# Performance work log

Hardware: AMD Instinct MI355X
Metric: run time of the kernel (lower is better)

## Reference

```python
import jax, jax.numpy as jnp
import numpy as np

B, Cin, Cout, H, W, K = 8, 256, 256, 64, 64, 3  # kernel 3x3, stride 1, pad 1, dilation 1
EPS = 1e-5


def setup_inputs() -> dict:
    key = jax.random.key(0)
    k0, k1, k2 = jax.random.split(key, 3)
    x = jax.random.normal(k0, (B, Cin, H, W), jnp.float32)
    # offset-predicting conv (mmcv zero-inits it; use small random weights so offsets are nontrivial)
    w_off = jax.random.normal(k1, (2 * K * K, Cin, K, K), jnp.float32) * 0.01
    b_off = jnp.zeros((2 * K * K,), jnp.float32)
    # main deformable conv weight
    w = jax.random.normal(k2, (Cout, Cin, K, K), jnp.float32) * (1.0 / np.sqrt(Cin * K * K))
    b = jnp.zeros((Cout,), jnp.float32)
    gamma = jnp.ones((Cout,), jnp.float32)
    beta = jnp.zeros((Cout,), jnp.float32)
    return {"x": x, "w_off": w_off, "b_off": b_off, "w": w, "b": b, "gamma": gamma, "beta": beta}


def _deform_fusion(x, w_off, b_off, w, b, gamma, beta):
    Bn, C, Hh, Ww = x.shape
    # 1) predict offsets: [B, 2*K*K, H, W]; channel layout is (dy, dx) per kernel tap
    offset = jax.lax.conv_general_dilated(x, w_off, (1, 1), ((1, 1), (1, 1)))
    offset = offset + b_off[None, :, None, None]
    off = offset.reshape(Bn, K * K, 2, Hh, Ww)
    dy, dx = off[:, :, 0], off[:, :, 1]  # each [B, K*K, H, W]

    # 2) sampling positions: p = p0 + p_k + delta_p  (stride 1, pad 1 -> p_k in {-1,0,1})
    kk = jnp.arange(K * K)
    ky = (kk // K - (K // 2)).astype(jnp.float32)[None, :, None, None]
    kx = (kk % K - (K // 2)).astype(jnp.float32)[None, :, None, None]
    py = ky + jnp.arange(Hh, dtype=jnp.float32)[None, None, :, None] + dy  # [B,K2,H,W]
    px = kx + jnp.arange(Ww, dtype=jnp.float32)[None, None, None, :] + dx

    # 3) bilinear sampling with zero padding outside the image
    y0 = jnp.floor(py); x0 = jnp.floor(px)
    fy = py - y0; fx = px - x0
    x_flat = x.reshape(Bn, C, Hh * Ww)

    def corner(yi, xi, wgt):
        valid = (yi >= 0) & (yi <= Hh - 1) & (xi >= 0) & (xi <= Ww - 1)
        idx = (jnp.clip(yi, 0, Hh - 1) * Ww + jnp.clip(xi, 0, Ww - 1)).astype(jnp.int32)
        idx = idx.reshape(Bn, -1)  # [B, K2*H*W]
        g = jax.vmap(lambda xf, ii: jnp.take(xf, ii, axis=1))(x_flat, idx)  # [B,C,K2*H*W]
        return g * (wgt * valid).reshape(Bn, 1, -1)

    sampled = (corner(y0,     x0,     (1 - fy) * (1 - fx))
             + corner(y0,     x0 + 1, (1 - fy) * fx)
             + corner(y0 + 1, x0,     fy * (1 - fx))
             + corner(y0 + 1, x0 + 1, fy * fx))  # [B, C, K2*H*W]
    sampled = sampled.reshape(Bn, C, K * K, Hh * Ww)

    # 4) contract sampled patches with conv weight: implicit-GEMM of deformable conv
    out = jnp.einsum('bckp,ock->bop', sampled, w.reshape(w.shape[0], C, K * K))
    out = out + b[None, :, None]
    out = out.reshape(Bn, -1, Hh, Ww)

    # 5) BatchNorm (training-mode batch statistics) + ReLU
    mean = out.mean(axis=(0, 2, 3), keepdims=True)
    var = out.var(axis=(0, 2, 3), keepdims=True)
    out = gamma[None, :, None, None] * (out - mean) * jax.lax.rsqrt(var + EPS) + beta[None, :, None, None]
    return jax.nn.relu(out)


def reference(x, w_off, b_off, w, b, gamma, beta):
    return _deform_fusion(x, w_off, b_off, w, b, gamma, beta)
```

## Files before the change

kernel.cpp:

```cpp
#include <hip/hip_runtime.h>
#include <math.h>

#define BN_ 8
#define CIN 256
#define COUT 256
#define HH 64
#define WW 64
#define HW 4096
#define KK 9
#define OC 18
#define EPS 1e-5f
#define NTOT (BN_ * COUT * HW)

#define OFF_WS 0
#define WTB_WS 589824
#define WOB_WS 884736
#define ST_WS  921600
#define XT_WS  922112

typedef float f32x4 __attribute__((ext_vector_type(4)));
typedef float f32x2 __attribute__((ext_vector_type(2)));
typedef short s16x8 __attribute__((ext_vector_type(8)));
typedef unsigned int u32x4 __attribute__((ext_vector_type(4)));

__device__ __forceinline__ unsigned short f2bf(float f) {
  unsigned int u = __float_as_uint(f);
  unsigned int r = (u + 0x7fffu + ((u >> 16) & 1u)) >> 16;
  return (unsigned short)r;
}
__device__ __forceinline__ float bf2f(short s) {
  return __uint_as_float(((unsigned int)(unsigned short)s) << 16);
}

__global__ __launch_bounds__(256) void xpose_kernel(
    const float* __restrict__ x, unsigned short* __restrict__ xt) {
  __shared__ float s[64][65];
  const int t = threadIdx.x;
  const int p0 = blockIdx.x * 64;
  const int c0 = blockIdx.y * 64;
  const int b  = blockIdx.z;
  const float* xb = x + ((size_t)b * CIN + c0) * HW + p0;
#pragma unroll
  for (int pass = 0; pass < 4; ++pass) {
    int cr = pass * 16 + (t >> 4);
    int ps = (t & 15) * 4;
    float4 v = *(const float4*)(xb + (size_t)cr * HW + ps);
    s[ps + 0][cr] = v.x; s[ps + 1][cr] = v.y; s[ps + 2][cr] = v.z; s[ps + 3][cr] = v.w;
  }
  __syncthreads();
  unsigned short* xo = xt + (size_t)b * 32 * HW * 8;
#pragma unroll
  for (int r = 0; r < 2; ++r) {
    int flat = r * 256 + t;
    int pr = flat >> 3, sub = flat & 7;
    int g8 = (c0 >> 3) + sub;
    s16x8 v;
#pragma unroll
    for (int j = 0; j < 8; ++j) v[j] = (short)f2bf(s[pr][sub * 8 + j]);
    *(s16x8*)(xo + ((size_t)g8 * HW + p0 + pr) * 8) = v;
  }
}

__global__ __launch_bounds__(256) void prep_kernel(
    const float* __restrict__ w_off, const float* __restrict__ w,
    unsigned short* __restrict__ wob, unsigned short* __restrict__ wTb,
    float* __restrict__ stats) {
  const int kb = blockIdx.x;
  const int kk = kb >> 3;
  const int c0 = (kb & 7) << 5;
  const int t = threadIdx.x;
  if (kb == 71) { stats[t] = 0.f; stats[256 + t] = 0.f; }
#pragma unroll
  for (int r = 0; r < 4; ++r) {
    int e = r * 256 + t;
    int g = e >> 8, m = (e >> 3) & 31, j = e & 7;
    int c = c0 + g * 8 + j;
    unsigned short v = 0;
    if (m < OC) v = f2bf(w_off[((size_t)m * CIN + c) * 9 + kk]);
    wob[(size_t)kb * 1024 + e] = v;
  }
#pragma unroll
  for (int g = 0; g < 4; ++g)
#pragma unroll
    for (int j = 0; j < 8; ++j) {
      int c = c0 + g * 8 + j;
      wTb[(((size_t)kb * 4 + g) * 256 + t) * 8 + j] =
          f2bf(w[((size_t)t * CIN + c) * 9 + kk]);
    }
}

__global__ __launch_bounds__(512, 4) void gemm_kernel(
    const unsigned short* __restrict__ xt, const unsigned short* __restrict__ wTb,
    const unsigned short* __restrict__ wob, const float* __restrict__ b_off,
    const float* __restrict__ bias, float* __restrict__ out,
    float* __restrict__ stats) {
  __shared__ __align__(16) char lds[73728];
  const int t = threadIdx.x;
  const int lane = t & 63;
  const int wv = t >> 6;
  const int b = blockIdx.x & 7;
  const int h = blockIdx.x >> 3;
  const int p0 = h * 64;
  const int col = t & 63;
  const int oct = t >> 6;
  const int fr = lane & 15, fq = lane >> 4;
  const unsigned short* xtb = xt + (size_t)b * 32 * HW * 8;
  float* s_off = (float*)(lds + 65536);
  unsigned short (*s_b)[4096] = (unsigned short(*)[4096])lds;

  {
    unsigned short* sb = (unsigned short*)lds + wv * 2048;
    f32x4 acc_o[2][4] = {};

    auto fetch = [&](int s, s16x8* V, s16x8* AF) {
      const int ki = wv * 9 + s;
      const int kk = ki >> 3, cc0g = (ki & 7) << 2;
      const int ky = kk / 3 - 1, kx = kk % 3 - 1;
      const int y = h + ky;
      const int xcol = lane + kx;
      const bool ok = (y >= 0) && (y < HH) && (xcol >= 0) && (xcol < WW);
      const int pix = y * WW + xcol;
#pragma unroll
      for (int g = 0; g < 4; ++g) {
        s16x8 v = {0, 0, 0, 0, 0, 0, 0, 0};
        if (ok)
          __builtin_memcpy(&v, (const char*)xtb + (((size_t)(cc0g + g)) << 16) + (size_t)pix * 16, 16);
        V[g] = v;
      }
      const unsigned short* ap = wob + (size_t)ki * 1024;
#pragma unroll
      for (int i = 0; i < 2; ++i)
        AF[i] = *(const s16x8*)&ap[(fq * 32 + i * 16 + fr) * 8];
    };

    s16x8 VE[4], VO[4], afE2[2], afO2[2];
    fetch(0, VE, afE2);

#define OBODY(S, VC, VN, AFC, AFN)                                             \
    {                                                                          \
      _Pragma("unroll")                                                        \
      for (int g = 0; g < 4; ++g)                                              \
        *(s16x8*)&sb[(g * 64 + lane) * 8] = VC[g];                             \
      if ((S) + 1 < 9) fetch((S) + 1, VN, AFN);                                \
      s16x8 bf[4];                                                             \
      _Pragma("unroll")                                                        \
      for (int jn = 0; jn < 4; ++jn)                                           \
        bf[jn] = *(const s16x8*)&sb[(fq * 64 + jn * 16 + fr) * 8];             \
      _Pragma("unroll")                                                        \
      for (int i = 0; i < 2; ++i)                                              \
        _Pragma("unroll")                                                      \
        for (int jn = 0; jn < 4; ++jn)                                         \
          acc_o[i][jn] = __builtin_amdgcn_mfma_f32_16x16x32_bf16(              \
              AFC[i], bf[jn], acc_o[i][jn], 0, 0, 0);                          \
    }

    for (int sp = 0; sp < 4; ++sp) {
      OBODY(2 * sp, VE, VO, afE2, afO2)
      OBODY(2 * sp + 1, VO, VE, afO2, afE2)
    }
    OBODY(8, VE, VO, afE2, afO2)
#undef OBODY

    __syncthreads();
    float* red = (float*)lds;
#pragma unroll
    for (int i = 0; i < 2; ++i)
#pragma unroll
      for (int jn = 0; jn < 4; ++jn)
#pragma unroll
        for (int rg = 0; rg < 4; ++rg)
          red[wv * 2048 + (i * 16 + fq * 4 + rg) * 64 + jn * 16 + fr] = acc_o[i][jn][rg];
    __syncthreads();

    const int e4 = t * 4;
    const int m = e4 >> 6;
    float4 v = make_float4(0.f, 0.f, 0.f, 0.f);
#pragma unroll
    for (int w = 0; w < 8; ++w) {
      float4 a = *(float4*)&red[w * 2048 + e4];
      v.x += a.x; v.y += a.y; v.z += a.z; v.w += a.w;
    }
    float bo = (m < OC) ? b_off[m] : 0.f;
    v.x += bo; v.y += bo; v.z += bo; v.w += bo;
    *(float4*)&s_off[e4] = v;
    __syncthreads();
  }

  int cofs[4];
  f32x2 qw2[4];

  auto calc = [&](int kk) {
    float dy = s_off[(2 * kk) * 64 + col];
    float dx = s_off[(2 * kk + 1) * 64 + col];
    float py = (float)(kk / 3 - 1 + h) + dy;
    float pxx = (float)(kk % 3 - 1 + col) + dx;
    float y0f = floorf(py), x0f = floorf(pxx);
    float fy = py - y0f, fx = pxx - x0f;
    int y0 = (int)y0f, x0 = (int)x0f;
    int y1 = y0 + 1, x1 = x0 + 1;
    bool vy0 = (y0 >= 0) && (y0 < HH), vy1 = (y1 >= 0) && (y1 < HH);
    bool vx0 = (x0 >= 0) && (x0 < WW), vx1 = (x1 >= 0) && (x1 < WW);
    int cy0 = min(max(y0, 0), HH - 1), cy1 = min(max(y1, 0), HH - 1);
    int cx0 = min(max(x0, 0), WW - 1), cx1 = min(max(x1, 0), WW - 1);
    float q0 = (vy0 && vx0) ? (1.f - fy) * (1.f - fx) : 0.f;
    float q1 = (vy0 && vx1) ? (1.f - fy) * fx : 0.f;
    float q2 = (vy1 && vx0) ? fy * (1.f - fx) : 0.f;
    float q3 = (vy1 && vx1) ? fy * fx : 0.f;
    cofs[0] = (cy0 * WW + cx0) * 16;  qw2[0][0] = q0; qw2[0][1] = q0;
    cofs[1] = (cy0 * WW + cx1) * 16;  qw2[1][0] = q1; qw2[1][1] = q1;
    cofs[2] = (cy1 * WW + cx0) * 16;  qw2[2][0] = q2; qw2[2][1] = q2;
    cofs[3] = (cy1 * WW + cx1) * 16;  qw2[3][0] = q3; qw2[3][1] = q3;
  };

  s16x8 g[4];

  auto gather = [&](int chunk64) {
    const char* bp = (const char*)xtb + (((size_t)(chunk64 * 8 + oct)) << 16);
#pragma unroll
    for (int k = 0; k < 4; ++k)
      __builtin_memcpy(&g[k], bp + cofs[k], 16);
  };

  auto combine_write = [&](int buf) {
    u32x4 vout;
#pragma unroll
    for (int jp = 0; jp < 4; ++jp) {
      f32x2 a = {0.f, 0.f};
#pragma unroll
      for (int k = 0; k < 4; ++k) {
        unsigned int pr = ((const unsigned int*)&g[k])[jp];
        f32x2 xv;
        xv[0] = __uint_as_float(pr << 16);
        xv[1] = __uint_as_float(pr & 0xffff0000u);
        a = __builtin_elementwise_fma(qw2[k], xv, a);
      }
      unsigned int packed;
      asm("v_cvt_pk_bf16_f32 %0, %1, %2" : "=v"(packed) : "v"(a[0]), "v"(a[1]));
      vout[jp] = packed;
    }
    *(u32x4*)&s_b[buf][(oct * 64 + col) * 8] = vout;
  };

  auto load_a = [&](int iter, s16x8 af[2][2]) {
#pragma unroll
    for (int ks = 0; ks < 2; ++ks) {
      const unsigned short* ap =
          wTb + (((size_t)(iter * 2 + ks) * 4 + fq) * 256 + wv * 32 + fr) * 8;
#pragma unroll
      for (int i = 0; i < 2; ++i)
        af[ks][i] = *(const s16x8*)(ap + (size_t)i * 16 * 8);
    }
  };

  f32x4 acc[2][4] = {};
  s16x8 afE[2][2], afO[2][2];

  {
    calc(0);
    gather(0);
    load_a(0, afE);
    combine_write(0);
  }
  asm volatile("s_waitcnt lgkmcnt(0)" ::: "memory");
  __builtin_amdgcn_s_barrier();

#define GBODY(I, AFC, AFN, CUR)                                                \
  {                                                                            \
    const int nx1 = (I) + 1;                                                   \
    if (nx1 < 36) {                                                            \
      if ((nx1 & 3) == 0) calc(nx1 >> 2);                                      \
      gather(nx1 & 3);                                                         \
      load_a(nx1, AFN);                                                        \
    }                                                                          \
    __builtin_amdgcn_s_setprio(1);                                             \
    _Pragma("unroll")                                                          \
    for (int ks = 0; ks < 2; ++ks)                                             \
      _Pragma("unroll")                                                        \
      for (int jj = 0; jj < 4; ++jj) {                                         \
        s16x8 bfr = *(const s16x8*)&s_b[CUR][((ks * 4 + fq) * 64 + jj * 16 + fr) * 8]; \
        _Pragma("unroll")                                                      \
        for (int ii = 0; ii < 2; ++ii)                                         \
          acc[ii][jj] = __builtin_amdgcn_mfma_f32_16x16x32_bf16(               \
              AFC[ks][ii], bfr, acc[ii][jj], 0, 0, 0);                         \
      }                                                                        \
    __builtin_amdgcn_s_setprio(0);                                             \
    if (nx1 < 36) {                                                            \
      combine_write((CUR) ^ 1);                                                \
      asm volatile("s_waitcnt lgkmcnt(0)" ::: "memory");                       \
      __builtin_amdgcn_s_barrier();                                            \
    }                                                                          \
  }

  for (int m = 0; m < 18; ++m) {
    const int i0 = 2 * m;
    GBODY(i0, afE, afO, 0)
    GBODY(i0 + 1, afO, afE, 1)
  }
#undef GBODY

#pragma unroll
  for (int i = 0; i < 2; ++i) {
#pragma unroll
    for (int rg = 0; rg < 4; ++rg) {
      int o = wv * 32 + i * 16 + fq * 4 + rg;
      float bv = bias[o];
      float* op = out + ((size_t)(b * COUT + o)) * HW + p0 + fr;
      float s = 0.f, s2 = 0.f;
#pragma unroll
      for (int j = 0; j < 4; ++j) {
        float val = acc[i][j][rg] + bv;
        op[j * 16] = val;
        s += val; s2 += val * val;
      }
#pragma unroll
      for (int m2 = 1; m2 < 16; m2 <<= 1) {
        s += __shfl_xor(s, m2);
        s2 += __shfl_xor(s2, m2);
      }
      if (fr == 0) {
        atomicAdd(&stats[o], s);
        atomicAdd(&stats[COUT + o], s2);
      }
    }
  }
}

__global__ __launch_bounds__(256) void bn_kernel(
    float* __restrict__ out, const float* __restrict__ stats,
    const float* __restrict__ gamma, const float* __restrict__ beta) {
  int i4 = (blockIdx.x * 256 + threadIdx.x) * 4;
  int o = (i4 >> 12) & (COUT - 1);
  const float inv_n = 1.f / (float)(BN_ * HW);
  float mean = stats[o] * inv_n;
  float var = stats[COUT + o] * inv_n - mean * mean;
  float sc = gamma[o] * rsqrtf(var + EPS);
  float sh = beta[o] - mean * sc;
  float4 v = *(float4*)(out + i4);
  v.x = fmaxf(fmaf(v.x, sc, sh), 0.f);
  v.y = fmaxf(fmaf(v.y, sc, sh), 0.f);
  v.z = fmaxf(fmaf(v.z, sc, sh), 0.f);
  v.w = fmaxf(fmaf(v.w, sc, sh), 0.f);
  *(float4*)(out + i4) = v;
}

extern "C" void kernel_launch(void* const* d_in, const int* in_sizes, int n_in,
                              void* d_out, int out_size, void* d_ws, size_t ws_size,
                              hipStream_t stream) {
  const float* x     = (const float*)d_in[0];
  const float* w_off = (const float*)d_in[1];
  const float* b_off = (const float*)d_in[2];
  const float* w     = (const float*)d_in[3];
  const float* bias  = (const float*)d_in[4];
  const float* gamma = (const float*)d_in[5];
  const float* beta  = (const float*)d_in[6];
  float* out = (float*)d_out;
  float* ws = (float*)d_ws;
  unsigned short* wTb = (unsigned short*)(ws + WTB_WS);
  unsigned short* wob = (unsigned short*)(ws + WOB_WS);
  float* stats = ws + ST_WS;
  unsigned short* xt = (unsigned short*)(ws + XT_WS);

  xpose_kernel<<<dim3(64, 4, 8), 256, 0, stream>>>(x, xt);
  prep_kernel<<<72, 256, 0, stream>>>(w_off, w, wob, wTb, stats);
  gemm_kernel<<<512, 512, 0, stream>>>(xt, wTb, wob, b_off, bias, out, stats);
  bn_kernel<<<NTOT / 1024, 256, 0, stream>>>(out, stats, gamma, beta);
}
```

Before: 213.7 us.

## Process two image rows per block with 1024 threads in the fused deform GEMM

Each block now covers two output rows (128 pixels) instead of one, using 16 waves and 256 blocks. Each wave owns 16 output channels across 128 pixels rather than 32 channels across 64 pixels. The offset-conv stage runs two passes, one per row half, and the shared sample buffer doubles. The aim is to halve the number of barrier-separated block iterations and amortize the weight loads over more pixels. In exchange, 256 blocks may underfill the CUs, LDS use grows, and launch_bounds(1024,4) is unrealistic and may constrain registers.

```diff
diff --git a/kernel.cpp b/kernel.cpp
--- a/kernel.cpp
+++ b/kernel.cpp
@@ -12,7 +12,6 @@
 #define EPS 1e-5f
 #define NTOT (BN_ * COUT * HW)
 
-#define OFF_WS 0
 #define WTB_WS 589824
 #define WOB_WS 884736
 #define ST_WS  921600
@@ -89,34 +88,37 @@
     }
 }
 
-__global__ __launch_bounds__(512, 4) void gemm_kernel(
+__global__ __launch_bounds__(1024, 4) void gemm_kernel(
     const unsigned short* __restrict__ xt, const unsigned short* __restrict__ wTb,
     const unsigned short* __restrict__ wob, const float* __restrict__ b_off,
     const float* __restrict__ bias, float* __restrict__ out,
     float* __restrict__ stats) {
-  __shared__ __align__(16) char lds[73728];
+  __shared__ __align__(16) char lds[81920];
   const int t = threadIdx.x;
   const int lane = t & 63;
   const int wv = t >> 6;
   const int b = blockIdx.x & 7;
-  const int h = blockIdx.x >> 3;
-  const int p0 = h * 64;
-  const int col = t & 63;
-  const int oct = t >> 6;
+  const int hh2 = blockIdx.x >> 3;
+  const int p0 = hh2 * 128;
+  const int col = t & 127;
+  const int oct = t >> 7;
   const int fr = lane & 15, fq = lane >> 4;
   const unsigned short* xtb = xt + (size_t)b * 32 * HW * 8;
   float* s_off = (float*)(lds + 65536);
-  unsigned short (*s_b)[4096] = (unsigned short(*)[4096])lds;
+  unsigned short (*s_b)[8192] = (unsigned short(*)[8192])lds;
 
   {
+    const int wg = wv & 7;
+    const int half = wv >> 3;
+    const int yrow = 2 * hh2 + half;
     unsigned short* sb = (unsigned short*)lds + wv * 2048;
     f32x4 acc_o[2][4] = {};
 
     auto fetch = [&](int s, s16x8* V, s16x8* AF) {
-      const int ki = wv * 9 + s;
+      const int ki = wg * 9 + s;
       const int kk = ki >> 3, cc0g = (ki & 7) << 2;
       const int ky = kk / 3 - 1, kx = kk % 3 - 1;
-      const int y = h + ky;
+      const int y = yrow + ky;
       const int xcol = lane + kx;
       const bool ok = (y >= 0) && (y < HH) && (xcol >= 0) && (xcol < WW);
       const int pix = y * WW + xcol;
@@ -164,36 +166,44 @@
     __syncthreads();
     float* red = (float*)lds;
 #pragma unroll
-    for (int i = 0; i < 2; ++i)
-#pragma unroll
-      for (int jn = 0; jn < 4; ++jn)
-#pragma unroll
-        for (int rg = 0; rg < 4; ++rg)
-          red[wv * 2048 + (i * 16 + fq * 4 + rg) * 64 + jn * 16 + fr] = acc_o[i][jn][rg];
-    __syncthreads();
-
-    const int e4 = t * 4;
-    const int m = e4 >> 6;
-    float4 v = make_float4(0.f, 0.f, 0.f, 0.f);
-#pragma unroll
-    for (int w = 0; w < 8; ++w) {
-      float4 a = *(float4*)&red[w * 2048 + e4];
-      v.x += a.x; v.y += a.y; v.z += a.z; v.w += a.w;
-    }
-    float bo = (m < OC) ? b_off[m] : 0.f;
-    v.x += bo; v.y += bo; v.z += bo; v.w += bo;
-    *(float4*)&s_off[e4] = v;
-    __syncthreads();
+    for (int pass = 0; pass < 2; ++pass) {
+      if (half == pass) {
+#pragma unroll
+        for (int i = 0; i < 2; ++i)
+#pragma unroll
+          for (int jn = 0; jn < 4; ++jn)
+#pragma unroll
+            for (int rg = 0; rg < 4; ++rg)
+              red[wg * 2048 + (i * 16 + fq * 4 + rg) * 64 + jn * 16 + fr] = acc_o[i][jn][rg];
+      }
+      __syncthreads();
+      {
+        const int f2 = t * 2;
+        const int m = f2 >> 6;
+        f32x2 v = {0.f, 0.f};
+#pragma unroll
+        for (int w = 0; w < 8; ++w) {
+          f32x2 a = *(f32x2*)&red[w * 2048 + f2];
+          v[0] += a[0]; v[1] += a[1];
+        }
+        float bo = (m < OC) ? b_off[m] : 0.f;
+        v[0] += bo; v[1] += bo;
+        *(f32x2*)&s_off[m * 128 + pass * 64 + (f2 & 63)] = v;
+      }
+      __syncthreads();
+    }
   }
 
   int cofs[4];
   f32x2 qw2[4];
 
   auto calc = [&](int kk) {
-    float dy = s_off[(2 * kk) * 64 + col];
-    float dx = s_off[(2 * kk + 1) * 64 + col];
-    float py = (float)(kk / 3 - 1 + h) + dy;
-    float pxx = (float)(kk % 3 - 1 + col) + dx;
+    float dy = s_off[(2 * kk) * 128 + col];
+    float dx = s_off[(2 * kk + 1) * 128 + col];
+    int y = 2 * hh2 + (col >> 6);
+    int xx = col & 63;
+    float py = (float)(kk / 3 - 1 + y) + dy;
+    float pxx = (float)(kk % 3 - 1 + xx) + dx;
     float y0f = floorf(py), x0f = floorf(pxx);
     float fy = py - y0f, fx = pxx - x0f;
     int y0 = (int)y0f, x0 = (int)x0f;
@@ -238,22 +248,17 @@
       asm("v_cvt_pk_bf16_f32 %0, %1, %2" : "=v"(packed) : "v"(a[0]), "v"(a[1]));
       vout[jp] = packed;
     }
-    *(u32x4*)&s_b[buf][(oct * 64 + col) * 8] = vout;
+    *(u32x4*)&s_b[buf][(oct * 128 + col) * 8] = vout;
   };
 
-  auto load_a = [&](int iter, s16x8 af[2][2]) {
-#pragma unroll
-    for (int ks = 0; ks < 2; ++ks) {
-      const unsigned short* ap =
-          wTb + (((size_t)(iter * 2 + ks) * 4 + fq) * 256 + wv * 32 + fr) * 8;
-#pragma unroll
-      for (int i = 0; i < 2; ++i)
-        af[ks][i] = *(const s16x8*)(ap + (size_t)i * 16 * 8);
-    }
+  auto load_a = [&](int iter, s16x8 af[2]) {
+#pragma unroll
+    for (int ks = 0; ks < 2; ++ks)
+      af[ks] = *(const s16x8*)&wTb[(((size_t)(iter * 2 + ks) * 4 + fq) * 256 + wv * 16 + fr) * 8];
   };
 
-  f32x4 acc[2][4] = {};
-  s16x8 afE[2][2], afO[2][2];
+  f32x4 acc[8] = {};
+  s16x8 afE[2], afO[2];
 
   {
     calc(0);
@@ -276,12 +281,10 @@
     _Pragma("unroll")                                                          \
     for (int ks = 0; ks < 2; ++ks)                                             \
       _Pragma("unroll")                                                        \
-      for (int jj = 0; jj < 4; ++jj) {                                         \
-        s16x8 bfr = *(const s16x8*)&s_b[CUR][((ks * 4 + fq) * 64 + jj * 16 + fr) * 8]; \
-        _Pragma("unroll")                                                      \
-        for (int ii = 0; ii < 2; ++ii)                                         \
-          acc[ii][jj] = __builtin_amdgcn_mfma_f32_16x16x32_bf16(               \
-              AFC[ks][ii], bfr, acc[ii][jj], 0, 0, 0);                         \
+      for (int jj = 0; jj < 8; ++jj) {                                         \
+        s16x8 bfr = *(const s16x8*)&s_b[CUR][((ks * 4 + fq) * 128 + jj * 16 + fr) * 8]; \
+        acc[jj] = __builtin_amdgcn_mfma_f32_16x16x32_bf16(                     \
+            AFC[ks], bfr, acc[jj], 0, 0, 0);                                   \
       }                                                                        \
     __builtin_amdgcn_s_setprio(0);                                             \
     if (nx1 < 36) {                                                            \
@@ -299,28 +302,25 @@
 #undef GBODY
 
 #pragma unroll
-  for (int i = 0; i < 2; ++i) {
-#pragma unroll
-    for (int rg = 0; rg < 4; ++rg) {
-      int o = wv * 32 + i * 16 + fq * 4 + rg;
-      float bv = bias[o];
-      float* op = out + ((size_t)(b * COUT + o)) * HW + p0 + fr;
-      float s = 0.f, s2 = 0.f;
-#pragma unroll
-      for (int j = 0; j < 4; ++j) {
-        float val = acc[i][j][rg] + bv;
-        op[j * 16] = val;
-        s += val; s2 += val * val;
-      }
-#pragma unroll
-      for (int m2 = 1; m2 < 16; m2 <<= 1) {
-        s += __shfl_xor(s, m2);
-        s2 += __shfl_xor(s2, m2);
-      }
-      if (fr == 0) {
-        atomicAdd(&stats[o], s);
-        atomicAdd(&stats[COUT + o], s2);
-      }
+  for (int rg = 0; rg < 4; ++rg) {
+    int o = wv * 16 + fq * 4 + rg;
+    float bv = bias[o];
+    float* op = out + ((size_t)(b * COUT + o)) * HW + p0 + fr;
+    float s = 0.f, s2 = 0.f;
+#pragma unroll
+    for (int j = 0; j < 8; ++j) {
+      float val = acc[j][rg] + bv;
+      op[j * 16] = val;
+      s += val; s2 += val * val;
+    }
+#pragma unroll
+    for (int m2 = 1; m2 < 16; m2 <<= 1) {
+      s += __shfl_xor(s, m2);
+      s2 += __shfl_xor(s2, m2);
+    }
+    if (fr == 0) {
+      atomicAdd(&stats[o], s);
+      atomicAdd(&stats[COUT + o], s2);
     }
   }
 }
@@ -362,6 +362,6 @@
 
   xpose_kernel<<<dim3(64, 4, 8), 256, 0, stream>>>(x, xt);
   prep_kernel<<<72, 256, 0, stream>>>(w_off, w, wob, wTb, stats);
-  gemm_kernel<<<512, 512, 0, stream>>>(xt, wTb, wob, b_off, bias, out, stats);
+  gemm_kernel<<<256, 1024, 0, stream>>>(xt, wTb, wob, b_off, bias, out, stats);
   bn_kernel<<<NTOT / 1024, 256, 0, stream>>>(out, stats, gamma, beta);
 }
```

Result: faster. 200.8 us (-6.1%).
